# Performance work log

Hardware: AMD Instinct MI355X
Metric: run time of the kernel (lower is better)

The kernel has to match this reference:

```python
import jax, jax.numpy as jnp
import numpy as np

F = 32          # field_size == len(feature_sizes) == mpl_dims[0]
V = 10000       # per-field vocab
D = 496         # embedding_size == comb(F, 2)
H = 1024        # mpl_dims[1]
OUT = 1         # mpl_dims[-1]
B = 16384


def setup_inputs() -> dict:
    key = jax.random.key(0)
    ks = jax.random.split(key, 8)
    xv = jax.random.normal(ks[0], (B, F), dtype=jnp.float32)
    xi = jax.random.randint(ks[1], (B, F), 0, V, dtype=jnp.int64)
    # stacked per-field embedding tables: [F, V, D]
    emb = jax.random.normal(ks[2], (F, V, D), dtype=jnp.float32) * 0.05
    W1 = jax.random.normal(ks[3], (F, H), dtype=jnp.float32) * (1.0 / np.sqrt(F))
    b1 = jax.random.normal(ks[4], (H,), dtype=jnp.float32) * 0.01
    W2 = jax.random.normal(ks[5], (H + D, OUT), dtype=jnp.float32) * (1.0 / np.sqrt(H + D))
    b2 = jax.random.normal(ks[6], (OUT,), dtype=jnp.float32) * 0.01
    return {"xv": xv, "xi": xi, "emb": emb, "W1": W1, "b1": b1, "W2": W2, "b2": b2}


def reference(xv, xi, emb, W1, b1, W2, b2):
    # Per-field embedding gather, scaled by the field value: e[b,f,:] = emb[f, xi[b,f], :] * xv[b,f]
    gathered = jax.vmap(lambda table, idx: table[idx], in_axes=(0, 1), out_axes=1)(emb, xi)  # [B, F, D]
    e = gathered * xv[:, :, None]
    # FM sum-square minus square-sum interaction -> [B, D]
    s = jnp.sum(e, axis=1)
    qi = 0.5 * (s * s - jnp.sum(e * e, axis=1))
    # MLP branch on raw values (dropout inactive at inference)
    h = jax.nn.relu(xv @ W1 + b1)  # [B, H]
    x = jnp.concatenate([qi, h], axis=1)  # [B, D + H]
    return x @ W2 + b2  # [B, OUT]
```

## Files before the change

kernel.cpp:

```cpp
#include <hip/hip_runtime.h>

constexpr int F  = 32;
constexpr int V  = 10000;
constexpr int D  = 496;
constexpr int H  = 1024;

__global__ __launch_bounds__(128, 8) void fm_kernel(
    const float* __restrict__ xv,
    const int*   __restrict__ xi,
    const float* __restrict__ emb,
    const float* __restrict__ W2,
    const float* __restrict__ b2,
    float* __restrict__ out)
{
    const int b = blockIdx.x;
    const int t = threadIdx.x;

    __shared__ float        s_xv[F];
    __shared__ const float* s_row[F];
    __shared__ float        s_wsum[2];

    if (t < F) {
        s_xv[t]  = xv[b * F + t];
        s_row[t] = emb + ((size_t)t * V + (size_t)xi[b * F + t]) * D;
    }
    __syncthreads();

    float acc = 0.0f;
    if (t < D / 4) {
        float4 s  = make_float4(0.f, 0.f, 0.f, 0.f);
        float4 ss = make_float4(0.f, 0.f, 0.f, 0.f);
        #pragma unroll 4
        for (int f = 0; f < F; ++f) {
            const float xf = s_xv[f];
            float4 v = *reinterpret_cast<const float4*>(s_row[f] + 4 * t);
            v.x *= xf; v.y *= xf; v.z *= xf; v.w *= xf;
            s.x  += v.x;       s.y  += v.y;       s.z  += v.z;       s.w  += v.w;
            ss.x += v.x * v.x; ss.y += v.y * v.y; ss.z += v.z * v.z; ss.w += v.w * v.w;
        }
        float4 w = *reinterpret_cast<const float4*>(W2 + 4 * t);
        acc = (0.5f * (s.x * s.x - ss.x)) * w.x
            + (0.5f * (s.y * s.y - ss.y)) * w.y
            + (0.5f * (s.z * s.z - ss.z)) * w.z
            + (0.5f * (s.w * s.w - ss.w)) * w.w;
    }

    #pragma unroll
    for (int off = 32; off > 0; off >>= 1)
        acc += __shfl_down(acc, off, 64);
    if ((t & 63) == 0) s_wsum[t >> 6] = acc;
    __syncthreads();
    if (t == 0) out[b] = s_wsum[0] + s_wsum[1] + b2[0];
}

constexpr int R  = 64;
constexpr int RC = 8;

__global__ __launch_bounds__(256, 4) void mlp_kernel(
    const float* __restrict__ xv,
    const float* __restrict__ W1,
    const float* __restrict__ b1,
    const float* __restrict__ W2,
    float* __restrict__ out,
    int B)
{
    const int t  = threadIdx.x;
    const int b0 = blockIdx.x * R;
    const int j0 = 4 * t;

    __shared__ float s_xv[F][R];
    __shared__ float s_red[RC][4];

    {
        const int r0 = t >> 3, f0 = 4 * (t & 7);
        const int rA = min(b0 + r0,      B - 1);
        const int rB = min(b0 + r0 + 32, B - 1);
        float4 v0 = *reinterpret_cast<const float4*>(xv + (size_t)rA * F + f0);
        float4 v1 = *reinterpret_cast<const float4*>(xv + (size_t)rB * F + f0);
        s_xv[f0 + 0][r0] = v0.x; s_xv[f0 + 1][r0] = v0.y;
        s_xv[f0 + 2][r0] = v0.z; s_xv[f0 + 3][r0] = v0.w;
        s_xv[f0 + 0][r0 + 32] = v1.x; s_xv[f0 + 1][r0 + 32] = v1.y;
        s_xv[f0 + 2][r0 + 32] = v1.z; s_xv[f0 + 3][r0 + 32] = v1.w;
    }
    __syncthreads();

    const float4 w2v = *reinterpret_cast<const float4*>(W2 + D + j0);
    const float4 bv  = *reinterpret_cast<const float4*>(b1 + j0);

    for (int rc = 0; rc < R; rc += RC) {
        float4 h[RC];
        #pragma unroll
        for (int r = 0; r < RC; ++r) h[r] = bv;

        #pragma unroll 4
        for (int f = 0; f < F; ++f) {
            const float4 w  = *reinterpret_cast<const float4*>(W1 + f * H + j0);
            const float4 xa = *reinterpret_cast<const float4*>(&s_xv[f][rc]);
            const float4 xb = *reinterpret_cast<const float4*>(&s_xv[f][rc + 4]);
            const float xr[RC] = {xa.x, xa.y, xa.z, xa.w, xb.x, xb.y, xb.z, xb.w};
            #pragma unroll
            for (int r = 0; r < RC; ++r) {
                h[r].x += xr[r] * w.x; h[r].y += xr[r] * w.y;
                h[r].z += xr[r] * w.z; h[r].w += xr[r] * w.w;
            }
        }

        #pragma unroll
        for (int r = 0; r < RC; ++r) {
            float p = fmaxf(h[r].x, 0.f) * w2v.x + fmaxf(h[r].y, 0.f) * w2v.y
                    + fmaxf(h[r].z, 0.f) * w2v.z + fmaxf(h[r].w, 0.f) * w2v.w;
            #pragma unroll
            for (int off = 32; off > 0; off >>= 1)
                p += __shfl_down(p, off, 64);
            if ((t & 63) == 0) s_red[r][t >> 6] = p;
        }
        __syncthreads();
        if (t < RC) {
            const int row = b0 + rc + t;
            if (row < B)
                out[row] += s_red[t][0] + s_red[t][1] + s_red[t][2] + s_red[t][3];
        }
        __syncthreads();
    }
}

extern "C" void kernel_launch(void* const* d_in, const int* in_sizes, int n_in,
                              void* d_out, int out_size, void* d_ws, size_t ws_size,
                              hipStream_t stream) {
    const float* xv  = (const float*)d_in[0];
    const int*   xi  = (const int*)d_in[1];
    const float* emb = (const float*)d_in[2];
    const float* W1  = (const float*)d_in[3];
    const float* b1  = (const float*)d_in[4];
    const float* W2  = (const float*)d_in[5];
    const float* b2  = (const float*)d_in[6];
    float* out = (float*)d_out;

    const int B = in_sizes[0] / F;

    fm_kernel<<<B, 128, 0, stream>>>(xv, xi, emb, W2, b2, out);
    mlp_kernel<<<(B + R - 1) / R, 256, 0, stream>>>(xv, W1, b1, W2, out, B);
}
```

Baseline: 880.2 us.

## Map one wavefront per batch row in FM kernel, four rows per block

```diff
diff --git a/kernel.cpp b/kernel.cpp
--- a/kernel.cpp
+++ b/kernel.cpp
@@ -5,52 +5,69 @@
 constexpr int D  = 496;
 constexpr int H  = 1024;
 
-__global__ __launch_bounds__(128, 8) void fm_kernel(
+__global__ __launch_bounds__(256, 6) void fm_kernel(
     const float* __restrict__ xv,
     const int*   __restrict__ xi,
     const float* __restrict__ emb,
     const float* __restrict__ W2,
     const float* __restrict__ b2,
-    float* __restrict__ out)
+    float* __restrict__ out,
+    int B)
 {
-    const int b = blockIdx.x;
-    const int t = threadIdx.x;
+    const int t  = threadIdx.x;
+    const int w  = t >> 6;
+    const int l  = t & 63;
+    const int b0 = blockIdx.x * 4;
 
-    __shared__ float        s_xv[F];
-    __shared__ const float* s_row[F];
-    __shared__ float        s_wsum[2];
+    __shared__ float        s_xv[4][F];
+    __shared__ const float* s_row[4][F];
 
-    if (t < F) {
-        s_xv[t]  = xv[b * F + t];
-        s_row[t] = emb + ((size_t)t * V + (size_t)xi[b * F + t]) * D;
+    if (t < 128) {
+        const int rr = t >> 5, f = t & 31;
+        const int r  = min(b0 + rr, B - 1);
+        s_xv[rr][f]  = xv[(size_t)r * F + f];
+        s_row[rr][f] = emb + ((size_t)f * V + (size_t)xi[(size_t)r * F + f]) * D;
     }
     __syncthreads();
 
-    float acc = 0.0f;
-    if (t < D / 4) {
-        float4 s  = make_float4(0.f, 0.f, 0.f, 0.f);
-        float4 ss = make_float4(0.f, 0.f, 0.f, 0.f);
-        #pragma unroll 4
-        for (int f = 0; f < F; ++f) {
-            const float xf = s_xv[f];
-            float4 v = *reinterpret_cast<const float4*>(s_row[f] + 4 * t);
-            v.x *= xf; v.y *= xf; v.z *= xf; v.w *= xf;
-            s.x  += v.x;       s.y  += v.y;       s.z  += v.z;       s.w  += v.w;
-            ss.x += v.x * v.x; ss.y += v.y * v.y; ss.z += v.z * v.z; ss.w += v.w * v.w;
-        }
-        float4 w = *reinterpret_cast<const float4*>(W2 + 4 * t);
-        acc = (0.5f * (s.x * s.x - ss.x)) * w.x
-            + (0.5f * (s.y * s.y - ss.y)) * w.y
-            + (0.5f * (s.z * s.z - ss.z)) * w.z
-            + (0.5f * (s.w * s.w - ss.w)) * w.w;
+    const int   c1 = (l < 60) ? l : 59;
+    const float m1 = (l < 60) ? 1.0f : 0.0f;
+
+    float4 s0  = make_float4(0.f, 0.f, 0.f, 0.f);
+    float4 ss0 = make_float4(0.f, 0.f, 0.f, 0.f);
+    float4 s1  = make_float4(0.f, 0.f, 0.f, 0.f);
+    float4 ss1 = make_float4(0.f, 0.f, 0.f, 0.f);
+
+    #pragma unroll 4
+    for (int f = 0; f < F; ++f) {
+        const float  xf = s_xv[w][f];
+        const float* p  = s_row[w][f];
+        float4 v0 = *reinterpret_cast<const float4*>(p + 4 * l);
+        float4 v1 = *reinterpret_cast<const float4*>(p + 256 + 4 * c1);
+        v0.x *= xf; v0.y *= xf; v0.z *= xf; v0.w *= xf;
+        v1.x *= xf; v1.y *= xf; v1.z *= xf; v1.w *= xf;
+        s0.x  += v0.x;        s0.y  += v0.y;        s0.z  += v0.z;        s0.w  += v0.w;
+        ss0.x += v0.x * v0.x; ss0.y += v0.y * v0.y; ss0.z += v0.z * v0.z; ss0.w += v0.w * v0.w;
+        s1.x  += v1.x;        s1.y  += v1.y;        s1.z  += v1.z;        s1.w  += v1.w;
+        ss1.x += v1.x * v1.x; ss1.y += v1.y * v1.y; ss1.z += v1.z * v1.z; ss1.w += v1.w * v1.w;
     }
+
+    const float4 w2a = *reinterpret_cast<const float4*>(W2 + 4 * l);
+    const float4 w2b = *reinterpret_cast<const float4*>(W2 + 256 + 4 * c1);
+
+    float acc = (0.5f * (s0.x * s0.x - ss0.x)) * w2a.x
+              + (0.5f * (s0.y * s0.y - ss0.y)) * w2a.y
+              + (0.5f * (s0.z * s0.z - ss0.z)) * w2a.z
+              + (0.5f * (s0.w * s0.w - ss0.w)) * w2a.w
+        + m1 * ((0.5f * (s1.x * s1.x - ss1.x)) * w2b.x
+              + (0.5f * (s1.y * s1.y - ss1.y)) * w2b.y
+              + (0.5f * (s1.z * s1.z - ss1.z)) * w2b.z
+              + (0.5f * (s1.w * s1.w - ss1.w)) * w2b.w);
 
     #pragma unroll
     for (int off = 32; off > 0; off >>= 1)
         acc += __shfl_down(acc, off, 64);
-    if ((t & 63) == 0) s_wsum[t >> 6] = acc;
-    __syncthreads();
-    if (t == 0) out[b] = s_wsum[0] + s_wsum[1] + b2[0];
+    if (l == 0 && b0 + w < B) out[b0 + w] = acc + b2[0];
 }
 
 constexpr int R  = 64;
@@ -138,6 +155,6 @@
 
     const int B = in_sizes[0] / F;
 
-    fm_kernel<<<B, 128, 0, stream>>>(xv, xi, emb, W2, b2, out);
+    fm_kernel<<<(B + 3) / 4, 256, 0, stream>>>(xv, xi, emb, W2, b2, out, B);
     mlp_kernel<<<(B + R - 1) / R, 256, 0, stream>>>(xv, W1, b1, W2, out, B);
 }
```

Measured after the change: 899.3 us. +2.2%, slower.
